# Kernel optimization log

Measured on AMD Instinct MI355X. Metric: run time of the kernel, lower is better.

Reference implementation:

```python
import jax, jax.numpy as jnp
import numpy as np

N_NODES = 50000
N_EDGES = 800000
H = 128   # atom_hidden_feats
B = 64    # bond_in_feats
NEG_SLOPE = 0.01  # torch LeakyReLU default


def setup_inputs() -> dict:
    key = jax.random.key(0)
    k1, k2, k3, k4, k5 = jax.random.split(key, 5)
    feat = jax.random.normal(k1, (N_NODES, H), dtype=jnp.float32)
    gdf_feat = jax.random.normal(k2, (N_EDGES, B), dtype=jnp.float32)
    # Linear(2H+B -> H): weight [H, 2H+B], bias [H]
    W = jax.random.normal(k3, (H, 2 * H + B), dtype=jnp.float32) * 0.05
    b = jnp.zeros((H,), dtype=jnp.float32)
    src = jax.random.randint(k4, (N_EDGES,), 0, N_NODES, dtype=jnp.int64)
    dst = jax.random.randint(k5, (N_EDGES,), 0, N_NODES, dtype=jnp.int64)
    return {"feat": feat, "gdf_feat": gdf_feat, "W": W, "b": b, "src": src, "dst": dst}


def reference(feat, gdf_feat, W, b, src, dst):
    n_nodes = feat.shape[0]
    # Per-edge message: concat(src_feat, dst_feat, edge_feat) -> linear -> gate
    z = jnp.concatenate([feat[src], feat[dst], gdf_feat], axis=-1)  # [E, 2H+B]
    z = z @ W.T + b                                                 # [E, H]
    msg = jax.nn.sigmoid(z) * jnp.where(z > 0, z, NEG_SLOPE * z)    # sigmoid * leaky_relu
    # Scatter-sum messages to destination nodes
    return jax.ops.segment_sum(msg, dst, num_segments=n_nodes)      # [N, H]
```

## Files before the change

kernel.cpp:

```cpp
#include <hip/hip_runtime.h>
#include <hip/hip_bf16.h>

typedef __attribute__((ext_vector_type(8)))  short bf16x8;
typedef __attribute__((ext_vector_type(16))) float f32x16;
typedef __attribute__((ext_vector_type(4)))  float f32x4;
typedef __attribute__((ext_vector_type(2)))  __fp16 fp16x2;

#define NN 50000
#define EE 800000
#define HH 128
#define KK 320
#define NEG 0.01f
#define NTILES (EE / 64)
#define NBLK 768

__device__ __forceinline__ unsigned pack2(float a, float b) {
    unsigned short lo = __builtin_bit_cast(unsigned short, __float2bfloat16(a));
    unsigned short hi = __builtin_bit_cast(unsigned short, __float2bfloat16(b));
    return (unsigned)lo | ((unsigned)hi << 16);
}

template<int USE_F16>
__global__ __launch_bounds__(256, 3) void fused_edge_kernel(
    const float* __restrict__ feat, const float* __restrict__ gdf,
    const float* __restrict__ W,    const float* __restrict__ bias,
    const int*   __restrict__ src,  const int*   __restrict__ dst,
    float* __restrict__ out, __fp16* __restrict__ acc16)
{
    __shared__ int4 lds4[64 * 40];
    __shared__ int  dsts[64];
    char* lds = (char*)lds4;

    const int tid  = threadIdx.x;
    const int lane = tid & 63;
    const int wid  = tid >> 6;
    const int col  = wid * 32 + (lane & 31);
    const int khalf = lane >> 5;
    const int r = tid >> 2, q = tid & 3;

    bf16x8 Wb[20];
    {
        const float* wrow = W + col * KK + khalf * 8;
        #pragma unroll
        for (int k = 0; k < 20; k++) {
            f32x4 x0 = *(const f32x4*)(wrow + k * 16);
            f32x4 x1 = *(const f32x4*)(wrow + k * 16 + 4);
            union { bf16x8 v; unsigned u[4]; } t;
            t.u[0] = pack2(x0[0], x0[1]); t.u[1] = pack2(x0[2], x0[3]);
            t.u[2] = pack2(x1[0], x1[1]); t.u[3] = pack2(x1[2], x1[3]);
            Wb[k] = t.v;
        }
    }
    const float bv = bias[col];

    int tile = blockIdx.x;
    int sCur = src[(long long)tile * 64 + r];
    int dCur = dst[(long long)tile * 64 + r];

    while (tile < NTILES) {
        const long long ebase = (long long)tile * 64;

        if (q == 0) dsts[r] = dCur;
        {
            const float* fs = feat + (long long)sCur * HH;
            const float* fd = feat + (long long)dCur * HH;
            const float* ge = gdf  + (ebase + r) * 64;
            #pragma unroll
            for (int i = 0; i < 10; i++) {
                const int c = q + i * 4;
                const float* p = (c < 16) ? (fs + c * 8)
                               : (c < 32) ? (fd + (c - 16) * 8)
                                          : (ge + (c - 32) * 8);
                f32x4 v0 = *(const f32x4*)p;
                f32x4 v1 = *(const f32x4*)(p + 4);
                int4 h;
                h.x = (int)pack2(v0[0], v0[1]); h.y = (int)pack2(v0[2], v0[3]);
                h.z = (int)pack2(v1[0], v1[1]); h.w = (int)pack2(v1[2], v1[3]);
                *(int4*)(lds + r * 640 + ((c * 16) ^ ((r & 7) << 4))) = h;
            }
        }
        __syncthreads();

        const int nt = tile + NBLK;
        if (nt < NTILES) {
            sCur = src[(long long)nt * 64 + r];
            dCur = dst[(long long)nt * 64 + r];
        }

        f32x16 acc0 = {}; f32x16 acc1 = {};
        const int arow = lane & 31;
        const int xr   = (arow & 7) << 4;
        #pragma unroll
        for (int k = 0; k < 20; k++) {
            const int kb = k * 32 + khalf * 16;
            bf16x8 a0 = *(const bf16x8*)(lds + arow * 640 + (kb ^ xr));
            bf16x8 a1 = *(const bf16x8*)(lds + (arow + 32) * 640 + (kb ^ xr));
            acc0 = __builtin_amdgcn_mfma_f32_32x32x16_bf16(a0, Wb[k], acc0, 0, 0, 0);
            acc1 = __builtin_amdgcn_mfma_f32_32x32x16_bf16(a1, Wb[k], acc1, 0, 0, 0);
        }

        #pragma unroll
        for (int rt = 0; rt < 2; rt++) {
            const f32x16 A = rt ? acc1 : acc0;
            #pragma unroll
            for (int g = 0; g < 4; g++) {
                #pragma unroll
                for (int j = 0; j < 4; j++) {
                    const int reg = g * 4 + j;
                    const int row = j + g * 8 + khalf * 4;
                    const float z  = A[reg] + bv;
                    const float lr = z > 0.f ? z : NEG * z;
                    const float sg = 1.f / (1.f + __expf(-z));
                    const float m  = lr * sg;
                    const int dn = dsts[rt * 32 + row];
                    if (USE_F16) {
                        const float o = __shfl_xor(m, 1);
                        if (!(lane & 1)) {
                            fp16x2 hv = __builtin_amdgcn_cvt_pkrtz(m, o);
                            __fp16* p = acc16 + (long long)dn * HH + col;
                            asm volatile("global_atomic_pk_add_f16 %0, %1, off"
                                         :: "v"(p), "v"(hv) : "memory");
                        }
                    } else {
                        unsafeAtomicAdd(out + (long long)dn * HH + col, m);
                    }
                }
            }
        }
        __syncthreads();
        tile = nt;
    }
}

__global__ __launch_bounds__(256) void conv_kernel(const int4* __restrict__ acc,
                                                   float4* __restrict__ out)
{
    const int i = blockIdx.x * 256 + threadIdx.x;
    union { int4 v; __fp16 h[8]; } u;
    u.v = acc[i];
    float4 a, b;
    a.x = (float)u.h[0]; a.y = (float)u.h[1]; a.z = (float)u.h[2]; a.w = (float)u.h[3];
    b.x = (float)u.h[4]; b.y = (float)u.h[5]; b.z = (float)u.h[6]; b.w = (float)u.h[7];
    out[2 * i]     = a;
    out[2 * i + 1] = b;
}

extern "C" void kernel_launch(void* const* d_in, const int* in_sizes, int n_in,
                              void* d_out, int out_size, void* d_ws, size_t ws_size,
                              hipStream_t stream) {
    const float* feat = (const float*)d_in[0];
    const float* gdf  = (const float*)d_in[1];
    const float* W    = (const float*)d_in[2];
    const float* bias = (const float*)d_in[3];
    const int*   src  = (const int*)d_in[4];
    const int*   dst  = (const int*)d_in[5];
    float* out = (float*)d_out;

    const size_t accBytes = (size_t)NN * HH * sizeof(__fp16);
    if (ws_size >= accBytes) {
        (void)hipMemsetAsync(d_ws, 0, accBytes, stream);
        fused_edge_kernel<1><<<NBLK, 256, 0, stream>>>(feat, gdf, W, bias, src, dst,
                                                       out, (__fp16*)d_ws);
        conv_kernel<<<(NN * HH / 8) / 256, 256, 0, stream>>>((const int4*)d_ws,
                                                             (float4*)out);
    } else {
        (void)hipMemsetAsync(out, 0, (size_t)out_size * sizeof(float), stream);
        fused_edge_kernel<0><<<NBLK, 256, 0, stream>>>(feat, gdf, W, bias, src, dst,
                                                       out, (__fp16*)d_ws);
    }
}
```

Measured before the change: 326.0 us.

## Pre-convert node features to bf16 so per-edge gathers fetch half the bytes

A new pre-pass kernel converts the node feature table to bf16 once per call and stores it in workspace. The fused edge kernel then gathers the source and destination rows as packed bf16, roughly halving the dominant random-gather traffic and dropping the per-edge conversion work. It also reads destination indices straight from global memory instead of staging them in LDS, raises the grid to 1024 blocks and the occupancy hint to 4. The trade-off is an extra conversion pass, a larger workspace requirement, and a final conversion block whose threads index past the end of the arrays.

```diff
diff --git a/kernel.cpp b/kernel.cpp
--- a/kernel.cpp
+++ b/kernel.cpp
@@ -12,7 +12,8 @@
 #define KK 320
 #define NEG 0.01f
 #define NTILES (EE / 64)
-#define NBLK 768
+#define NBLK 1024
+#define ACC_BYTES ((size_t)NN * HH * 2)
 
 __device__ __forceinline__ unsigned pack2(float a, float b) {
     unsigned short lo = __builtin_bit_cast(unsigned short, __float2bfloat16(a));
@@ -20,15 +21,28 @@
     return (unsigned)lo | ((unsigned)hi << 16);
 }
 
-template<int USE_F16>
-__global__ __launch_bounds__(256, 3) void fused_edge_kernel(
-    const float* __restrict__ feat, const float* __restrict__ gdf,
-    const float* __restrict__ W,    const float* __restrict__ bias,
-    const int*   __restrict__ src,  const int*   __restrict__ dst,
+__global__ __launch_bounds__(256) void featcvt_kernel(const float* __restrict__ feat,
+                                                      ushort* __restrict__ featb)
+{
+    const int t = blockIdx.x * 256 + threadIdx.x;
+    const float* p = feat + (long long)t * 8;
+    f32x4 v0 = *(const f32x4*)p;
+    f32x4 v1 = *(const f32x4*)(p + 4);
+    int4 h;
+    h.x = (int)pack2(v0[0], v0[1]); h.y = (int)pack2(v0[2], v0[3]);
+    h.z = (int)pack2(v1[0], v1[1]); h.w = (int)pack2(v1[2], v1[3]);
+    *(int4*)(featb + (long long)t * 8) = h;
+}
+
+template<int USE_F16, int FEATB>
+__global__ __launch_bounds__(256, 4) void fused_edge_kernel(
+    const float*  __restrict__ feat, const ushort* __restrict__ featb,
+    const float*  __restrict__ gdf,
+    const float*  __restrict__ W,    const float* __restrict__ bias,
+    const int*    __restrict__ src,  const int*   __restrict__ dst,
     float* __restrict__ out, __fp16* __restrict__ acc16)
 {
     __shared__ int4 lds4[64 * 40];
-    __shared__ int  dsts[64];
     char* lds = (char*)lds4;
 
     const int tid  = threadIdx.x;
@@ -60,23 +74,45 @@
     while (tile < NTILES) {
         const long long ebase = (long long)tile * 64;
 
-        if (q == 0) dsts[r] = dCur;
         {
-            const float* fs = feat + (long long)sCur * HH;
-            const float* fd = feat + (long long)dCur * HH;
-            const float* ge = gdf  + (ebase + r) * 64;
-            #pragma unroll
-            for (int i = 0; i < 10; i++) {
-                const int c = q + i * 4;
-                const float* p = (c < 16) ? (fs + c * 8)
-                               : (c < 32) ? (fd + (c - 16) * 8)
-                                          : (ge + (c - 32) * 8);
-                f32x4 v0 = *(const f32x4*)p;
-                f32x4 v1 = *(const f32x4*)(p + 4);
-                int4 h;
-                h.x = (int)pack2(v0[0], v0[1]); h.y = (int)pack2(v0[2], v0[3]);
-                h.z = (int)pack2(v1[0], v1[1]); h.w = (int)pack2(v1[2], v1[3]);
-                *(int4*)(lds + r * 640 + ((c * 16) ^ ((r & 7) << 4))) = h;
+            const float* ge = gdf + (ebase + r) * 64;
+            if (FEATB) {
+                const ushort* fs = featb + (long long)sCur * HH;
+                const ushort* fd = featb + (long long)dCur * HH;
+                #pragma unroll
+                for (int i = 0; i < 8; i++) {
+                    const int c = q + i * 4;
+                    const ushort* p = (c < 16) ? (fs + c * 8) : (fd + (c - 16) * 8);
+                    int4 h = *(const int4*)p;
+                    *(int4*)(lds + r * 640 + ((c * 16) ^ ((r & 7) << 4))) = h;
+                }
+                #pragma unroll
+                for (int i = 8; i < 10; i++) {
+                    const int c = q + i * 4;
+                    const float* p = ge + (c - 32) * 8;
+                    f32x4 v0 = *(const f32x4*)p;
+                    f32x4 v1 = *(const f32x4*)(p + 4);
+                    int4 h;
+                    h.x = (int)pack2(v0[0], v0[1]); h.y = (int)pack2(v0[2], v0[3]);
+                    h.z = (int)pack2(v1[0], v1[1]); h.w = (int)pack2(v1[2], v1[3]);
+                    *(int4*)(lds + r * 640 + ((c * 16) ^ ((r & 7) << 4))) = h;
+                }
+            } else {
+                const float* fs = feat + (long long)sCur * HH;
+                const float* fd = feat + (long long)dCur * HH;
+                #pragma unroll
+                for (int i = 0; i < 10; i++) {
+                    const int c = q + i * 4;
+                    const float* p = (c < 16) ? (fs + c * 8)
+                                   : (c < 32) ? (fd + (c - 16) * 8)
+                                              : (ge + (c - 32) * 8);
+                    f32x4 v0 = *(const f32x4*)p;
+                    f32x4 v1 = *(const f32x4*)(p + 4);
+                    int4 h;
+                    h.x = (int)pack2(v0[0], v0[1]); h.y = (int)pack2(v0[2], v0[3]);
+                    h.z = (int)pack2(v1[0], v1[1]); h.w = (int)pack2(v1[2], v1[3]);
+                    *(int4*)(lds + r * 640 + ((c * 16) ^ ((r & 7) << 4))) = h;
+                }
             }
         }
         __syncthreads();
@@ -99,6 +135,7 @@
             acc1 = __builtin_amdgcn_mfma_f32_32x32x16_bf16(a1, Wb[k], acc1, 0, 0, 0);
         }
 
+        const int* dtile = dst + ebase;
         #pragma unroll
         for (int rt = 0; rt < 2; rt++) {
             const f32x16 A = rt ? acc1 : acc0;
@@ -112,7 +149,7 @@
                     const float lr = z > 0.f ? z : NEG * z;
                     const float sg = 1.f / (1.f + __expf(-z));
                     const float m  = lr * sg;
-                    const int dn = dsts[rt * 32 + row];
+                    const int dn = dtile[rt * 32 + row];
                     if (USE_F16) {
                         const float o = __shfl_xor(m, 1);
                         if (!(lane & 1)) {
@@ -156,16 +193,25 @@
     const int*   dst  = (const int*)d_in[5];
     float* out = (float*)d_out;
 
-    const size_t accBytes = (size_t)NN * HH * sizeof(__fp16);
-    if (ws_size >= accBytes) {
-        (void)hipMemsetAsync(d_ws, 0, accBytes, stream);
-        fused_edge_kernel<1><<<NBLK, 256, 0, stream>>>(feat, gdf, W, bias, src, dst,
-                                                       out, (__fp16*)d_ws);
+    __fp16* acc16 = (__fp16*)d_ws;
+    ushort* featb = (ushort*)((char*)d_ws + ACC_BYTES);
+
+    if (ws_size >= 2 * ACC_BYTES) {
+        (void)hipMemsetAsync(d_ws, 0, ACC_BYTES, stream);
+        featcvt_kernel<<<(NN * HH / 8) / 256 + 1, 256, 0, stream>>>(feat, featb);
+        fused_edge_kernel<1, 1><<<NBLK, 256, 0, stream>>>(feat, featb, gdf, W, bias,
+                                                          src, dst, out, acc16);
+        conv_kernel<<<(NN * HH / 8) / 256, 256, 0, stream>>>((const int4*)d_ws,
+                                                             (float4*)out);
+    } else if (ws_size >= ACC_BYTES) {
+        (void)hipMemsetAsync(d_ws, 0, ACC_BYTES, stream);
+        fused_edge_kernel<1, 0><<<NBLK, 256, 0, stream>>>(feat, featb, gdf, W, bias,
+                                                          src, dst, out, acc16);
         conv_kernel<<<(NN * HH / 8) / 256, 256, 0, stream>>>((const int4*)d_ws,
                                                              (float4*)out);
     } else {
         (void)hipMemsetAsync(out, 0, (size_t)out_size * sizeof(float), stream);
-        fused_edge_kernel<0><<<NBLK, 256, 0, stream>>>(feat, gdf, W, bias, src, dst,
-                                                       out, (__fp16*)d_ws);
+        fused_edge_kernel<0, 0><<<NBLK, 256, 0, stream>>>(feat, featb, gdf, W, bias,
+                                                          src, dst, out, acc16);
     }
 }
```

Result: slower. 395.2 us (+21.2%).
